# Performance work log

Measured on AMD Instinct MI355X. Metric: run time of the kernel, lower is better.

Reference implementation:

```python
import jax, jax.numpy as jnp
import numpy as np

N = 50000   # nodes
E = 800000  # edges (avg degree 16)
D = 128     # feature dim (input = hidden = output)
EPS = 1e-6


def setup_inputs() -> dict:
    key = jax.random.key(0)
    ks = jax.random.split(key, 8)
    xav = np.sqrt(6.0 / (D + D)).astype(np.float32)  # xavier_uniform bound for [D,D]
    inp = {
        "x": jax.random.normal(ks[0], (N, D), dtype=jnp.float32),
        "edge_index": jax.random.randint(ks[1], (2, E), 0, N, dtype=jnp.int64),
    }
    for i in range(3):
        inp[f"W{i+1}"] = jax.random.uniform(ks[2 + i], (D, D), dtype=jnp.float32, minval=-xav, maxval=xav)
        inp[f"b{i+1}"] = jnp.zeros((D,), dtype=jnp.float32)
        inp[f"g{i+1}"] = jnp.ones((D,), dtype=jnp.float32)   # RMSNorm gain
    return inp


def _rmsnorm(x, g):
    # x: [N, D]
    return x * jax.lax.rsqrt(jnp.mean(x * x, axis=-1, keepdims=True) + EPS) * g


def _gcn_layer(x, src, dst, edge_norm, W, b):
    # x: [N, D_in] -> [N, D_out]; sparse gather-scatter over edges (incl. self-loops)
    h = x @ W                                   # [N, D_out]
    msg = h[src] * edge_norm[:, None]           # gather + scale, [E+N, D_out]
    agg = jax.ops.segment_sum(msg, dst, num_segments=N)  # scatter-add, [N, D_out]
    return agg + b


def reference(x, edge_index, W1, b1, g1, W2, b2, g2, W3, b3, g3):
    # GCNConv default: add self-loops, symmetric D^{-1/2}(A+I)D^{-1/2} normalization
    loop = jnp.arange(N, dtype=edge_index.dtype)
    src = jnp.concatenate([edge_index[0], loop])  # [E+N]
    dst = jnp.concatenate([edge_index[1], loop])  # [E+N]
    deg = jax.ops.segment_sum(jnp.ones_like(dst, dtype=x.dtype), dst, num_segments=N)
    dinv = jnp.where(deg > 0, jax.lax.rsqrt(jnp.maximum(deg, 1.0)), 0.0)
    edge_norm = dinv[src] * dinv[dst]             # [E+N]

    for W, b, g in ((W1, b1, g1), (W2, b2, g2), (W3, b3, g3)):
        h = _rmsnorm(x, g)                         # pre-norm
        x = jax.nn.relu(_gcn_layer(h, src, dst, edge_norm, W, b))
    return x
```

## Files before the change

### kernel.cpp

```cpp
#include <hip/hip_runtime.h>
#include <cstdint>
#include <cstddef>

#define NN 50000
#define EE 800000
#define DD 128
#define NBLK 196


using bf16x8 = __attribute__((ext_vector_type(8))) short;
using f32x4  = __attribute__((ext_vector_type(4))) float;

__device__ __forceinline__ unsigned int f2bf(float f) {
    unsigned int u = __float_as_uint(f);
    u += 0x7fffu + ((u >> 16) & 1u);
    return u >> 16;
}
__device__ __forceinline__ float bf2f(unsigned int hi) { return __uint_as_float(hi << 16); }
__device__ __forceinline__ float bflo(unsigned int u) { return __uint_as_float(u << 16); }
__device__ __forceinline__ float bfhi(unsigned int u) { return __uint_as_float(u & 0xffff0000u); }

__device__ __forceinline__ int ld_idx(const int* __restrict__ p, long long i, int mode64) {
    return mode64 ? p[2 * i] : p[(size_t)i];
}

__global__ void probe_kernel(const int* __restrict__ ei, int* __restrict__ flag) {
    int t = threadIdx.x;
    int v = ei[2 * t + 1];
    unsigned long long b = __ballot(v != 0);
    if (t == 0) *flag = (b == 0ull) ? 1 : 0;
}

__global__ void count_kernel(const int* __restrict__ ei, const int* __restrict__ flag,
                             int* __restrict__ deg, int* __restrict__ rank) {
    int e = blockIdx.x * 256 + threadIdx.x;
    if (e >= EE) return;
    int m = *flag;
    int d = ld_idx(ei, (long long)EE + e, m);
    rank[e] = atomicAdd(&deg[d], 1);
}

__global__ __launch_bounds__(256) void partial_kernel(const int* __restrict__ deg,
                                                      int* __restrict__ bsum) {
    int idx = blockIdx.x * 256 + threadIdx.x;
    int v = (idx < NN) ? deg[idx] : 0;
    for (int off = 1; off < 64; off <<= 1) v += __shfl_xor(v, off);
    __shared__ int ws[4];
    if ((threadIdx.x & 63) == 0) ws[threadIdx.x >> 6] = v;
    __syncthreads();
    if (threadIdx.x == 0) bsum[blockIdx.x] = ws[0] + ws[1] + ws[2] + ws[3];
}

__global__ __launch_bounds__(256) void bscan_kernel(const int* __restrict__ bsum,
                                                    int* __restrict__ boff) {
    __shared__ int sh[256];
    int t = threadIdx.x;
    sh[t] = (t < NBLK) ? bsum[t] : 0;
    __syncthreads();
    for (int off = 1; off < 256; off <<= 1) {
        int u = (t >= off) ? sh[t - off] : 0;
        __syncthreads();
        sh[t] += u;
        __syncthreads();
    }
    if (t <= NBLK) boff[t] = (t == 0) ? 0 : sh[t - 1];
}

__global__ __launch_bounds__(256) void scatter_scan_kernel(
        const int* __restrict__ deg, const int* __restrict__ boff,
        int* __restrict__ row_ptr, float* __restrict__ dinv) {
    __shared__ int sh[256];
    int t = threadIdx.x;
    int idx = blockIdx.x * 256 + t;
    int v = (idx < NN) ? deg[idx] : 0;
    sh[t] = v;
    __syncthreads();
    for (int off = 1; off < 256; off <<= 1) {
        int u = (t >= off) ? sh[t - off] : 0;
        __syncthreads();
        sh[t] += u;
        __syncthreads();
    }
    if (idx < NN) {
        row_ptr[idx] = boff[blockIdx.x] + sh[t] - v;
        dinv[idx] = rsqrtf((float)(v + 1));
    }
    if (idx == 0) row_ptr[NN] = boff[NBLK];
}

__global__ void fill_kernel(const int* __restrict__ ei, const int* __restrict__ flag,
                            const int* __restrict__ row_ptr, const int* __restrict__ rank,
                            const float* __restrict__ dinv, uint2* __restrict__ csr) {
    int e = blockIdx.x * 256 + threadIdx.x;
    if (e >= EE) return;
    int m = *flag;
    int sv = ld_idx(ei, (long long)e, m);
    int dv = ld_idx(ei, (long long)EE + e, m);
    int pos = row_ptr[dv] + rank[e];
    csr[pos] = make_uint2((unsigned)sv, __float_as_uint(dinv[sv]));
}

__global__ __launch_bounds__(256) void convw_kernel(const float* __restrict__ W,
        unsigned short* __restrict__ WhT, unsigned short* __restrict__ WlT) {
    int id = blockIdx.x * 256 + threadIdx.x;
    int k = id >> 7, n = id & 127;
    float w = W[id];
    unsigned int hi = f2bf(w);
    unsigned int lo = f2bf(w - bf2f(hi));
    WhT[n * 128 + k] = (unsigned short)hi;
    WlT[n * 128 + k] = (unsigned short)lo;
}

__global__ __launch_bounds__(256) void rmsnorm_mfma_kernel(
        const float* __restrict__ X, const unsigned short* __restrict__ WhT,
        const unsigned short* __restrict__ WlT, const float* __restrict__ g,
        uint4* __restrict__ H) {
    __shared__ uint4 smem[2048];
    int t = threadIdx.x;
    int row0 = blockIdx.x * 64;

    int r = t >> 2, part = t & 3;
    int row = row0 + r;
    float4 v[8];
    float ss = 0.f;
    if (row < NN) {
        const float4* xr = (const float4*)(X + (size_t)row * DD) + part * 8;
        #pragma unroll
        for (int i = 0; i < 8; i++) {
            v[i] = xr[i];
            ss += v[i].x * v[i].x + v[i].y * v[i].y + v[i].z * v[i].z + v[i].w * v[i].w;
        }
    } else {
        #pragma unroll
        for (int i = 0; i < 8; i++) v[i] = make_float4(0.f, 0.f, 0.f, 0.f);
    }
    ss += __shfl_xor(ss, 1);
    ss += __shfl_xor(ss, 2);
    float sc = rsqrtf(ss * (1.0f / DD) + 1e-6f);

    const float4* g4 = (const float4*)g + part * 8;
    #pragma unroll
    for (int c = 0; c < 4; c++) {
        float f[8];
        #pragma unroll
        for (int h = 0; h < 2; h++) {
            float4 gq = g4[2 * c + h];
            float4 xv = v[2 * c + h];
            f[4 * h + 0] = xv.x * sc * gq.x;
            f[4 * h + 1] = xv.y * sc * gq.y;
            f[4 * h + 2] = xv.z * sc * gq.z;
            f[4 * h + 3] = xv.w * sc * gq.w;
        }
        unsigned int hb[8], lb[8];
        #pragma unroll
        for (int j = 0; j < 8; j++) {
            hb[j] = f2bf(f[j]);
            lb[j] = f2bf(f[j] - bf2f(hb[j]));
        }
        uint4 hq, lq;
        hq.x = hb[0] | (hb[1] << 16); hq.y = hb[2] | (hb[3] << 16);
        hq.z = hb[4] | (hb[5] << 16); hq.w = hb[6] | (hb[7] << 16);
        lq.x = lb[0] | (lb[1] << 16); lq.y = lb[2] | (lb[3] << 16);
        lq.z = lb[4] | (lb[5] << 16); lq.w = lb[6] | (lb[7] << 16);
        int idx = r * 16 + ((part * 4 + c) ^ (r & 7));
        smem[idx] = hq;
        smem[1024 + idx] = lq;
    }
    __syncthreads();

    int w = t >> 6, lane = t & 63;
    int kg = lane >> 4;
    int arow = w * 16 + (lane & 15);
    bf16x8 ah[4], al[4];
    #pragma unroll
    for (int kk = 0; kk < 4; kk++) {
        int idx = arow * 16 + ((kk * 4 + kg) ^ (arow & 7));
        ah[kk] = *(const bf16x8*)&smem[idx];
        al[kk] = *(const bf16x8*)&smem[1024 + idx];
    }
    __syncthreads();

    const bf16x8* whv = (const bf16x8*)WhT;
    const bf16x8* wlv = (const bf16x8*)WlT;
    f32x4 acc[8];
    #pragma unroll
    for (int nt = 0; nt < 8; nt++) acc[nt] = (f32x4){0.f, 0.f, 0.f, 0.f};
    #pragma unroll
    for (int nt = 0; nt < 8; nt++) {
        int bi = (nt * 16 + (lane & 15)) * 16 + kg;
        #pragma unroll
        for (int kk = 0; kk < 4; kk++) {
            bf16x8 bh = whv[bi + kk * 4];
            bf16x8 bl = wlv[bi + kk * 4];
            acc[nt] = __builtin_amdgcn_mfma_f32_16x16x32_bf16(ah[kk], bh, acc[nt], 0, 0, 0);
            acc[nt] = __builtin_amdgcn_mfma_f32_16x16x32_bf16(al[kk], bh, acc[nt], 0, 0, 0);
            acc[nt] = __builtin_amdgcn_mfma_f32_16x16x32_bf16(ah[kk], bl, acc[nt], 0, 0, 0);
        }
    }

    unsigned short* hsm = (unsigned short*)smem;
    #pragma unroll
    for (int nt = 0; nt < 8; nt++) {
        #pragma unroll
        for (int q = 0; q < 4; q++) {
            int rr = w * 16 + (lane >> 4) * 4 + q;
            int cc = nt * 16 + (lane & 15);
            hsm[rr * 128 + cc] = (unsigned short)f2bf(acc[nt][q]);
        }
    }
    __syncthreads();
    if (row < NN) {
        #pragma unroll
        for (int c = 0; c < 4; c++)
            H[(size_t)row * 16 + part * 4 + c] = smem[r * 16 + part * 4 + c];
    }
}

__global__ __launch_bounds__(256) void aggregate_kernel(
        const unsigned int* __restrict__ Hm, const float* __restrict__ dinv,
        const int* __restrict__ row_ptr, const uint2* __restrict__ csr,
        const float* __restrict__ b, float* __restrict__ out) {
    __shared__ uint2 sEdge[4][64];
    int wv = threadIdx.x >> 6;
    int lane = threadIdx.x & 63;
    int n = blockIdx.x * 4 + wv;
    int grp = lane >> 4;
    int tc = lane & 15;
    const uint4* H4 = (const uint4*)Hm;
    float dn = dinv[n];
    float acc[8];
    #pragma unroll
    for (int i = 0; i < 8; i++) acc[i] = 0.f;

    if (grp == 0) {
        uint4 q = H4[(size_t)n * 16 + tc];
        float w = dn * dn;
        const float4* b4 = (const float4*)b;
        float4 ba = b4[2 * tc], bb = b4[2 * tc + 1];
        acc[0] = fmaf(bflo(q.x), w, ba.x);
        acc[1] = fmaf(bfhi(q.x), w, ba.y);
        acc[2] = fmaf(bflo(q.y), w, ba.z);
        acc[3] = fmaf(bfhi(q.y), w, ba.w);
        acc[4] = fmaf(bflo(q.z), w, bb.x);
        acc[5] = fmaf(bfhi(q.z), w, bb.y);
        acc[6] = fmaf(bflo(q.w), w, bb.z);
        acc[7] = fmaf(bfhi(q.w), w, bb.w);
    }

    int start = row_ptr[n], end = row_ptr[n + 1];
    for (int base = start; base < end; base += 64) {
        int m = min(64, end - base);
        if (lane < m) sEdge[wv][lane] = csr[base + lane];
        int j = grp;
        for (; j + 4 < m; j += 8) {
            uint2 p0 = sEdge[wv][j];
            uint2 p1 = sEdge[wv][j + 4];
            uint4 q0 = H4[(size_t)p0.x * 16 + tc];
            uint4 q1 = H4[(size_t)p1.x * 16 + tc];
            float w0 = __uint_as_float(p0.y) * dn;
            float w1 = __uint_as_float(p1.y) * dn;
            acc[0] = fmaf(bflo(q0.x), w0, acc[0]);
            acc[1] = fmaf(bfhi(q0.x), w0, acc[1]);
            acc[2] = fmaf(bflo(q0.y), w0, acc[2]);
            acc[3] = fmaf(bfhi(q0.y), w0, acc[3]);
            acc[4] = fmaf(bflo(q0.z), w0, acc[4]);
            acc[5] = fmaf(bfhi(q0.z), w0, acc[5]);
            acc[6] = fmaf(bflo(q0.w), w0, acc[6]);
            acc[7] = fmaf(bfhi(q0.w), w0, acc[7]);
            acc[0] = fmaf(bflo(q1.x), w1, acc[0]);
            acc[1] = fmaf(bfhi(q1.x), w1, acc[1]);
            acc[2] = fmaf(bflo(q1.y), w1, acc[2]);
            acc[3] = fmaf(bfhi(q1.y), w1, acc[3]);
            acc[4] = fmaf(bflo(q1.z), w1, acc[4]);
            acc[5] = fmaf(bfhi(q1.z), w1, acc[5]);
            acc[6] = fmaf(bflo(q1.w), w1, acc[6]);
            acc[7] = fmaf(bfhi(q1.w), w1, acc[7]);
        }
        if (j < m) {
            uint2 p = sEdge[wv][j];
            uint4 q = H4[(size_t)p.x * 16 + tc];
            float w = __uint_as_float(p.y) * dn;
            acc[0] = fmaf(bflo(q.x), w, acc[0]);
            acc[1] = fmaf(bfhi(q.x), w, acc[1]);
            acc[2] = fmaf(bflo(q.y), w, acc[2]);
            acc[3] = fmaf(bfhi(q.y), w, acc[3]);
            acc[4] = fmaf(bflo(q.z), w, acc[4]);
            acc[5] = fmaf(bfhi(q.z), w, acc[5]);
            acc[6] = fmaf(bflo(q.w), w, acc[6]);
            acc[7] = fmaf(bfhi(q.w), w, acc[7]);
        }
    }

    #pragma unroll
    for (int i = 0; i < 8; i++) {
        acc[i] += __shfl_xor(acc[i], 16);
        acc[i] += __shfl_xor(acc[i], 32);
    }
    if (grp == 0) {
        float4 o0, o1;
        o0.x = fmaxf(acc[0], 0.f); o0.y = fmaxf(acc[1], 0.f);
        o0.z = fmaxf(acc[2], 0.f); o0.w = fmaxf(acc[3], 0.f);
        o1.x = fmaxf(acc[4], 0.f); o1.y = fmaxf(acc[5], 0.f);
        o1.z = fmaxf(acc[6], 0.f); o1.w = fmaxf(acc[7], 0.f);
        float4* orow = (float4*)(out + (size_t)n * DD + 8 * tc);
        orow[0] = o0;
        orow[1] = o1;
    }
}

extern "C" void kernel_launch(void* const* d_in, const int* in_sizes, int n_in,
                              void* d_out, int out_size, void* d_ws, size_t ws_size,
                              hipStream_t stream) {
    (void)in_sizes; (void)n_in; (void)out_size; (void)ws_size;
    const float* x  = (const float*)d_in[0];
    const int*   ei = (const int*)d_in[1];
    const float* W1 = (const float*)d_in[2];
    const float* b1 = (const float*)d_in[3];
    const float* g1 = (const float*)d_in[4];
    const float* W2 = (const float*)d_in[5];
    const float* b2 = (const float*)d_in[6];
    const float* g2 = (const float*)d_in[7];
    const float* W3 = (const float*)d_in[8];
    const float* b3 = (const float*)d_in[9];
    const float* g3 = (const float*)d_in[10];
    float* out = (float*)d_out;

    char* wsb = (char*)d_ws;
    int*   deg     = (int*)(wsb + 0);
    int*   bsum    = (int*)(wsb + 200000);
    int*   boff    = (int*)(wsb + 200832);
    int*   row_ptr = (int*)(wsb + 400000);
    int*   rank    = (int*)(wsb + 600064);
    float* dinv    = (float*)(wsb + 3800064);
    int*   flag    = (int*)(wsb + 4000064);
    unsigned int* Hb = (unsigned int*)(wsb + 4000256);
    uint2* csr     = (uint2*)(wsb + 16800256);
    unsigned short* WhT = (unsigned short*)(wsb + 23200256);
    unsigned short* WlT = (unsigned short*)(wsb + 23233024);

    hipMemsetAsync(deg, 0, 200000, stream);

    probe_kernel<<<1, 64, 0, stream>>>(ei, flag);
    count_kernel<<<(EE + 255) / 256, 256, 0, stream>>>(ei, flag, deg, rank);
    partial_kernel<<<NBLK, 256, 0, stream>>>(deg, bsum);
    bscan_kernel<<<1, 256, 0, stream>>>(bsum, boff);
    scatter_scan_kernel<<<NBLK, 256, 0, stream>>>(deg, boff, row_ptr, dinv);
    fill_kernel<<<(EE + 255) / 256, 256, 0, stream>>>(ei, flag, row_ptr, rank, dinv, csr);

    const int gemm_grid = (NN + 63) / 64;
    const int agg_grid  = NN / 4;
    uint4* H4 = (uint4*)Hb;

    convw_kernel<<<64, 256, 0, stream>>>(W1, WhT, WlT);
    rmsnorm_mfma_kernel<<<gemm_grid, 256, 0, stream>>>(x, WhT, WlT, g1, H4);
    aggregate_kernel<<<agg_grid, 256, 0, stream>>>(Hb, dinv, row_ptr, csr, b1, out);

    convw_kernel<<<64, 256, 0, stream>>>(W2, WhT, WlT);
    rmsnorm_mfma_kernel<<<gemm_grid, 256, 0, stream>>>(out, WhT, WlT, g2, H4);
    aggregate_kernel<<<agg_grid, 256, 0, stream>>>(Hb, dinv, row_ptr, csr, b2, out);

    convw_kernel<<<64, 256, 0, stream>>>(W3, WhT, WlT);
    rmsnorm_mfma_kernel<<<gemm_grid, 256, 0, stream>>>(out, WhT, WlT, g3, H4);
    aggregate_kernel<<<agg_grid, 256, 0, stream>>>(Hb, dinv, row_ptr, csr, b3, out);
}
```

Baseline: 375.8 us.

## Batch weight conversion into one launch and widen GEMM blocks to 512 threads

The three per-layer weight split/transpose launches become one kernel that converts W1..W3 together at the start. The fused RMSNorm+MFMA GEMM kernel now uses 512 threads per 64-row tile: 8 threads per row for the norm, and 8 waves split 4x2 over rows and column halves, so each wave does half as many MFMAs. The bf16 output staging in shared memory is padded to a row stride of 136 to reduce bank conflicts on the write-back. The goal is fewer launches and more waves per tile to hide latency, at the cost of each wave reloading the A fragments and more shared-memory traffic per block.

After: 362.0 us. 3.7% less time.

```diff
diff --git a/kernel.cpp b/kernel.cpp
--- a/kernel.cpp
+++ b/kernel.cpp
@@ -100,18 +100,24 @@
     csr[pos] = make_uint2((unsigned)sv, __float_as_uint(dinv[sv]));
 }
 
-__global__ __launch_bounds__(256) void convw_kernel(const float* __restrict__ W,
+__global__ __launch_bounds__(256) void convw3_kernel(
+        const float* __restrict__ W1, const float* __restrict__ W2,
+        const float* __restrict__ W3,
         unsigned short* __restrict__ WhT, unsigned short* __restrict__ WlT) {
     int id = blockIdx.x * 256 + threadIdx.x;
-    int k = id >> 7, n = id & 127;
-    float w = W[id];
+    int layer = id >> 14;
+    int i = id & 16383;
+    const float* W = (layer == 0) ? W1 : (layer == 1) ? W2 : W3;
+    int k = i >> 7, n = i & 127;
+    float w = W[i];
     unsigned int hi = f2bf(w);
     unsigned int lo = f2bf(w - bf2f(hi));
-    WhT[n * 128 + k] = (unsigned short)hi;
-    WlT[n * 128 + k] = (unsigned short)lo;
-}
-
-__global__ __launch_bounds__(256) void rmsnorm_mfma_kernel(
+    WhT[layer * 16384 + n * 128 + k] = (unsigned short)hi;
+    WlT[layer * 16384 + n * 128 + k] = (unsigned short)lo;
+}
+
+#define HSTR 136
+__global__ __launch_bounds__(512) void rmsnorm_mfma_kernel(
         const float* __restrict__ X, const unsigned short* __restrict__ WhT,
         const unsigned short* __restrict__ WlT, const float* __restrict__ g,
         uint4* __restrict__ H) {
@@ -119,28 +125,29 @@
     int t = threadIdx.x;
     int row0 = blockIdx.x * 64;
 
-    int r = t >> 2, part = t & 3;
+    int r = t >> 3, part = t & 7;
     int row = row0 + r;
-    float4 v[8];
+    float4 v[4];
     float ss = 0.f;
     if (row < NN) {
-        const float4* xr = (const float4*)(X + (size_t)row * DD) + part * 8;
-        #pragma unroll
-        for (int i = 0; i < 8; i++) {
+        const float4* xr = (const float4*)(X + (size_t)row * DD) + part * 4;
+        #pragma unroll
+        for (int i = 0; i < 4; i++) {
             v[i] = xr[i];
             ss += v[i].x * v[i].x + v[i].y * v[i].y + v[i].z * v[i].z + v[i].w * v[i].w;
         }
     } else {
         #pragma unroll
-        for (int i = 0; i < 8; i++) v[i] = make_float4(0.f, 0.f, 0.f, 0.f);
+        for (int i = 0; i < 4; i++) v[i] = make_float4(0.f, 0.f, 0.f, 0.f);
     }
     ss += __shfl_xor(ss, 1);
     ss += __shfl_xor(ss, 2);
+    ss += __shfl_xor(ss, 4);
     float sc = rsqrtf(ss * (1.0f / DD) + 1e-6f);
 
-    const float4* g4 = (const float4*)g + part * 8;
-    #pragma unroll
-    for (int c = 0; c < 4; c++) {
+    const float4* g4 = (const float4*)g + part * 4;
+    #pragma unroll
+    for (int c = 0; c < 2; c++) {
         float f[8];
         #pragma unroll
         for (int h = 0; h < 2; h++) {
@@ -162,15 +169,17 @@
         hq.z = hb[4] | (hb[5] << 16); hq.w = hb[6] | (hb[7] << 16);
         lq.x = lb[0] | (lb[1] << 16); lq.y = lb[2] | (lb[3] << 16);
         lq.z = lb[4] | (lb[5] << 16); lq.w = lb[6] | (lb[7] << 16);
-        int idx = r * 16 + ((part * 4 + c) ^ (r & 7));
+        int ch = part * 2 + c;
+        int idx = r * 16 + (ch ^ (r & 7));
         smem[idx] = hq;
         smem[1024 + idx] = lq;
     }
     __syncthreads();
 
     int w = t >> 6, lane = t & 63;
+    int wr = w & 3, wc = w >> 2;
     int kg = lane >> 4;
-    int arow = w * 16 + (lane & 15);
+    int arow = wr * 16 + (lane & 15);
     bf16x8 ah[4], al[4];
     #pragma unroll
     for (int kk = 0; kk < 4; kk++) {
@@ -182,12 +191,12 @@
 
     const bf16x8* whv = (const bf16x8*)WhT;
     const bf16x8* wlv = (const bf16x8*)WlT;
-    f32x4 acc[8];
-    #pragma unroll
-    for (int nt = 0; nt < 8; nt++) acc[nt] = (f32x4){0.f, 0.f, 0.f, 0.f};
-    #pragma unroll
-    for (int nt = 0; nt < 8; nt++) {
-        int bi = (nt * 16 + (lane & 15)) * 16 + kg;
+    f32x4 acc[4];
+    #pragma unroll
+    for (int nt = 0; nt < 4; nt++) acc[nt] = (f32x4){0.f, 0.f, 0.f, 0.f};
+    #pragma unroll
+    for (int nt = 0; nt < 4; nt++) {
+        int bi = (wc * 64 + nt * 16 + (lane & 15)) * 16 + kg;
         #pragma unroll
         for (int kk = 0; kk < 4; kk++) {
             bf16x8 bh = whv[bi + kk * 4];
@@ -200,19 +209,22 @@
 
     unsigned short* hsm = (unsigned short*)smem;
     #pragma unroll
-    for (int nt = 0; nt < 8; nt++) {
+    for (int nt = 0; nt < 4; nt++) {
         #pragma unroll
         for (int q = 0; q < 4; q++) {
-            int rr = w * 16 + (lane >> 4) * 4 + q;
-            int cc = nt * 16 + (lane & 15);
-            hsm[rr * 128 + cc] = (unsigned short)f2bf(acc[nt][q]);
+            int rr = wr * 16 + (lane >> 4) * 4 + q;
+            int cc = wc * 64 + nt * 16 + (lane & 15);
+            hsm[rr * HSTR + cc] = (unsigned short)f2bf(acc[nt][q]);
         }
     }
     __syncthreads();
     if (row < NN) {
-        #pragma unroll
-        for (int c = 0; c < 4; c++)
-            H[(size_t)row * 16 + part * 4 + c] = smem[r * 16 + part * 4 + c];
+        const uint4* hsm4 = (const uint4*)smem;
+        #pragma unroll
+        for (int c = 0; c < 2; c++) {
+            int ch = part * 2 + c;
+            H[(size_t)row * 16 + ch] = hsm4[r * 17 + ch];
+        }
     }
 }
 
@@ -336,10 +348,11 @@
     unsigned int* Hb = (unsigned int*)(wsb + 4000256);
     uint2* csr     = (uint2*)(wsb + 16800256);
     unsigned short* WhT = (unsigned short*)(wsb + 23200256);
-    unsigned short* WlT = (unsigned short*)(wsb + 23233024);
+    unsigned short* WlT = (unsigned short*)(wsb + 23298560);
 
     hipMemsetAsync(deg, 0, 200000, stream);
 
+    convw3_kernel<<<192, 256, 0, stream>>>(W1, W2, W3, WhT, WlT);
     probe_kernel<<<1, 64, 0, stream>>>(ei, flag);
     count_kernel<<<(EE + 255) / 256, 256, 0, stream>>>(ei, flag, deg, rank);
     partial_kernel<<<NBLK, 256, 0, stream>>>(deg, bsum);
@@ -351,15 +364,10 @@
     const int agg_grid  = NN / 4;
     uint4* H4 = (uint4*)Hb;
 
-    convw_kernel<<<64, 256, 0, stream>>>(W1, WhT, WlT);
-    rmsnorm_mfma_kernel<<<gemm_grid, 256, 0, stream>>>(x, WhT, WlT, g1, H4);
+    rmsnorm_mfma_kernel<<<gemm_grid, 512, 0, stream>>>(x, WhT, WlT, g1, H4);
     aggregate_kernel<<<agg_grid, 256, 0, stream>>>(Hb, dinv, row_ptr, csr, b1, out);
-
-    convw_kernel<<<64, 256, 0, stream>>>(W2, WhT, WlT);
-    rmsnorm_mfma_kernel<<<gemm_grid, 256, 0, stream>>>(out, WhT, WlT, g2, H4);
+    rmsnorm_mfma_kernel<<<gemm_grid, 512, 0, stream>>>(out, WhT + 16384, WlT + 16384, g2, H4);
     aggregate_kernel<<<agg_grid, 256, 0, stream>>>(Hb, dinv, row_ptr, csr, b2, out);
-
-    convw_kernel<<<64, 256, 0, stream>>>(W3, WhT, WlT);
-    rmsnorm_mfma_kernel<<<gemm_grid, 256, 0, stream>>>(out, WhT, WlT, g3, H4);
+    rmsnorm_mfma_kernel<<<gemm_grid, 512, 0, stream>>>(out, WhT + 32768, WlT + 32768, g3, H4);
     aggregate_kernel<<<agg_grid, 256, 0, stream>>>(Hb, dinv, row_ptr, csr, b3, out);
 }
```
